# Performance work log

Hardware: AMD Instinct MI355X
Metric: run time of the kernel (lower is better)

Reference implementation:

```python
import jax, jax.numpy as jnp
import numpy as np

B, I, H = 8192, 1024, 2048
G = 2            # number of groups
WR = 256         # wRank
URANKS = [128, 128]


def setup_inputs() -> dict:
    key = jax.random.key(0)
    ks = jax.random.split(key, 7)
    Hg = H // G
    x = jax.random.normal(ks[0], (B, I), jnp.float32)
    h = jax.random.normal(ks[1], (B, H), jnp.float32)
    c = jax.random.normal(ks[2], (B, H), jnp.float32)
    W = 0.1 * jax.random.normal(ks[3], (I, WR), jnp.float32)
    # Ws[k]: (wRank, H) for k in {forget, input, out, gate}
    Ws = 0.1 * jax.random.normal(ks[4], (4, WR, H), jnp.float32)
    # Ug[idx][0]: (G, H/G, r) shared first factor per rotation idx
    U0 = 0.1 * jax.random.normal(ks[5], (len(URANKS), G, Hg, URANKS[0]), jnp.float32)
    # Ug[idx][1..4]: (G, r, H/G) per-gate second factors, order [f, i, o, g]
    Ugates = 0.1 * jax.random.normal(ks[6], (len(URANKS), 4, G, URANKS[0], Hg), jnp.float32)
    # biases init to ones in the original module; order [f, i, o, c]
    biases = jnp.ones((4, H), jnp.float32)
    return {"x": x, "h": h, "c": c, "W": W, "Ws": Ws,
            "U0": U0, "Ugates": Ugates, "biases": biases}


def _cell(x, h, c, W, Ws, U0, Ugates, biases):
    Bb, Hh = h.shape
    Hg = Hh // G
    # shared input projection: x @ W, then all 4 gate matrices at once
    xw = x @ W                                   # (B, WR)
    wVals = jnp.einsum('br,krh->kbh', xw, Ws)    # (4, B, H)
    hview = h.reshape(Bb, G, Hg)                 # (B, G, H/G)
    uVals = jnp.zeros_like(wVals)
    for idx in range(U0.shape[0]):
        # group rotation: index = [idx, idx+1, ..., 0, ..., idx-1]
        rolled = jnp.roll(hview, -idx, axis=1)                     # (B, G, H/G)
        t = jnp.einsum('bgk,gkr->bgr', rolled, U0[idx])            # shared first bmm
        uVals = uVals + jnp.einsum('bgr,fgrk->fbgk', t, Ugates[idx]).reshape(4, Bb, Hh)
    pre = wVals + uVals + biases[:, None, :]     # (4, B, H)
    f = jax.nn.sigmoid(pre[0])
    i = jax.nn.sigmoid(pre[1])
    o = jax.nn.sigmoid(pre[2])
    g = jnp.tanh(pre[3])
    c_next = f * c + i * g
    h_next = o * jnp.tanh(c_next)
    return c_next, h_next


def reference(x, h, c, W, Ws, U0, Ugates, biases):
    return _cell(x, h, c, W, Ws, U0, Ugates, biases)
```

## Files before the change

### kernel.cpp

```cpp
#include <hip/hip_runtime.h>
#include <math.h>


typedef _Float16 half_t;
typedef _Float16 half8 __attribute__((ext_vector_type(8)));
typedef float floatx4 __attribute__((ext_vector_type(4)));

#define MFMA16(a, b, c) __builtin_amdgcn_mfma_f32_16x16x32_f16((a), (b), (c), 0, 0, 0)

typedef __attribute__((address_space(3))) unsigned int lds_uint;
typedef __attribute__((address_space(1))) const unsigned int glb_uint;

__device__ __forceinline__ void gload_lds16(const void* gptr, void* ldsptr) {
    __builtin_amdgcn_global_load_lds((glb_uint*)gptr, (lds_uint*)ldsptr, 16, 0, 0);
}

__device__ __forceinline__ int swz_ro(int row, int lq) {
    return row * 32 + ((lq ^ ((row >> 1) & 3)) << 3);
}

#define OFF_VTH  0u
#define OFF_VTL  4194304u
#define OFF_WTH  8388608u
#define OFF_WTL  8650752u
#define OFF_U0TH 8912896u
#define OFF_U0TL 9437184u
#define OFF_ZH   9961472u
#define OFF_ZL   16252928u

__global__ void prep_Vt(const float* __restrict__ Ws, const float* __restrict__ Ug,
                        half_t* __restrict__ Vth, half_t* __restrict__ Vtl) {
    __shared__ half_t Lh[16][520];
    __shared__ half_t Ll[16][520];
    const int b   = blockIdx.x;
    const int f   = b & 3;
    const int hc4 = (b >> 2) & 3;
    const int hc6 = (b >> 4) & 15;
    const int g   = b >> 8;
    const int t   = threadIdx.x;
    const int kk  = t >> 4;
    const int hcl = t & 15;
    const int n   = hc6 * 64 + hc4 * 16 + hcl;

    for (int p = 0; p < 32; ++p) {
        const int k = p * 16 + kk;
        float v;
        if (k < 256)
            v = Ws[((size_t)f * 256 + k) * 2048 + g * 1024 + n];
        else if (k < 384)
            v = Ug[(((size_t)f * 2 + g) * 128 + (k - 256)) * 1024 + n];
        else
            v = Ug[(((size_t)(4 + f) * 2 + g) * 128 + (k - 384)) * 1024 + n];
        const half_t hi = (half_t)v;
        Lh[hcl][k] = hi;
        Ll[hcl][k] = (half_t)(v - (float)hi);
    }
    __syncthreads();
    const int rl = t >> 4;
    const int ch = (t & 15) * 32;
    const size_t R0 = (size_t)b * 16;
    half_t* dh = Vth + (R0 + rl) * 512 + ch;
    half_t* dl = Vtl + (R0 + rl) * 512 + ch;
#pragma unroll
    for (int j = 0; j < 4; ++j) {
        *(half8*)&dh[j * 8] = *(const half8*)&Lh[rl][ch + j * 8];
        *(half8*)&dl[j * 8] = *(const half8*)&Ll[rl][ch + j * 8];
    }
}

__global__ void prep_ABw(const float* __restrict__ W, const float* __restrict__ U0,
                         half_t* __restrict__ Wth, half_t* __restrict__ Wtl,
                         half_t* __restrict__ U0th, half_t* __restrict__ U0tl) {
    __shared__ half_t Lh[8][1040];
    __shared__ half_t Ll[8][1040];
    const int rb  = blockIdx.x;
    const int tgt = blockIdx.y;
    const int t   = threadIdx.x;
    const int kk  = t >> 3;
    const int rl  = t & 7;
    const int r   = rb * 8 + rl;

    for (int p = 0; p < 32; ++p) {
        const int k = p * 32 + kk;
        float v;
        if (tgt == 0) {
            v = W[(size_t)k * 256 + r];
        } else {
            const int jj = tgt - 1;
            if (r < 128) v = U0[((size_t)jj * 1024 + k) * 128 + r];
            else         v = U0[((size_t)(2 + (1 - jj)) * 1024 + k) * 128 + (r - 128)];
        }
        const half_t hi = (half_t)v;
        Lh[rl][k] = hi;
        Ll[rl][k] = (half_t)(v - (float)hi);
    }
    __syncthreads();
    const int orl = t >> 5;
    const int ch  = (t & 31) * 32;
    half_t *dh, *dl;
    if (tgt == 0) { dh = Wth; dl = Wtl; }
    else { dh = U0th + (size_t)(tgt - 1) * 262144; dl = U0tl + (size_t)(tgt - 1) * 262144; }
    dh += (size_t)(rb * 8 + orl) * 1024 + ch;
    dl += (size_t)(rb * 8 + orl) * 1024 + ch;
#pragma unroll
    for (int j = 0; j < 4; ++j) {
        *(half8*)&dh[j * 8] = *(const half8*)&Lh[orl][ch + j * 8];
        *(half8*)&dl[j * 8] = *(const half8*)&Ll[orl][ch + j * 8];
    }
}

__global__ __launch_bounds__(256, 2) void stageA_mfma(
    const float* __restrict__ x, const float* __restrict__ h,
    const half_t* __restrict__ Wth, const half_t* __restrict__ Wtl,
    const half_t* __restrict__ U0th, const half_t* __restrict__ U0tl,
    half_t* __restrict__ Zh, half_t* __restrict__ Zl) {
    __shared__ half_t Ah[64 * 32], Al[64 * 32];
    __shared__ half_t Bh[256 * 32], Bl[256 * 32];
    const int m0  = blockIdx.x * 64;
    const int seg = blockIdx.y;
    const int tid = threadIdx.x;
    const int l   = tid & 63, wid = tid >> 6;
    const int wr  = wid >> 1, wcn = wid & 1;

    const float* Asrc; int ldA;
    if (seg == 0) { Asrc = x; ldA = 1024; }
    else          { Asrc = h + (seg - 1) * 1024; ldA = 2048; }
    const half_t *Bsh, *Bsl;
    if (seg == 0) { Bsh = Wth; Bsl = Wtl; }
    else { Bsh = U0th + (size_t)(seg - 1) * 262144; Bsl = U0tl + (size_t)(seg - 1) * 262144; }

    const int arow = tid >> 2, au = tid & 3;
    const int aqp  = (au ^ ((tid >> 3) & 3));
    const float* aptr = Asrc + (size_t)(m0 + arow) * ldA + au * 8;
    const int lrow = l >> 2;
    const int lks  = ((l & 3) ^ ((l >> 3) & 3)) << 3;

    floatx4 acc[2][8] = {};

#pragma unroll 1
    for (int kt = 0; kt < 1024; kt += 32) {
        __syncthreads();
        const float4 v0 = *(const float4*)(aptr + kt);
        const float4 v1 = *(const float4*)(aptr + kt + 4);
        const float va[8] = {v0.x, v0.y, v0.z, v0.w, v1.x, v1.y, v1.z, v1.w};
        half8 hv, lv;
#pragma unroll
        for (int j = 0; j < 8; ++j) {
            const half_t hi = (half_t)va[j];
            hv[j] = hi;
            lv[j] = (half_t)(va[j] - (float)hi);
        }
        *(half8*)&Ah[arow * 32 + aqp * 8] = hv;
        *(half8*)&Al[arow * 32 + aqp * 8] = lv;
#pragma unroll
        for (int q = 0; q < 4; ++q) {
            const int i = wid * 4 + q;
            const size_t grow = (size_t)(i * 16 + lrow) * 1024 + kt + lks;
            gload_lds16(Bsh + grow, &Bh[i * 512]);
            gload_lds16(Bsl + grow, &Bl[i * 512]);
        }
        __syncthreads();

        half8 ah[2], al[2];
#pragma unroll
        for (int mt = 0; mt < 2; ++mt) {
            const int ro = swz_ro(wr * 32 + mt * 16 + (l & 15), l >> 4);
            ah[mt] = *(const half8*)&Ah[ro];
            al[mt] = *(const half8*)&Al[ro];
        }
#pragma unroll
        for (int nt = 0; nt < 8; ++nt) {
            const int ro = swz_ro(wcn * 128 + nt * 16 + (l & 15), l >> 4);
            const half8 bh = *(const half8*)&Bh[ro];
            const half8 bl = *(const half8*)&Bl[ro];
#pragma unroll
            for (int mt = 0; mt < 2; ++mt) {
                acc[mt][nt] = MFMA16(ah[mt], bh, acc[mt][nt]);
                acc[mt][nt] = MFMA16(ah[mt], bl, acc[mt][nt]);
                acc[mt][nt] = MFMA16(al[mt], bh, acc[mt][nt]);
            }
        }
    }
#pragma unroll
    for (int mt = 0; mt < 2; ++mt)
#pragma unroll
        for (int nt = 0; nt < 8; ++nt)
#pragma unroll
            for (int r = 0; r < 4; ++r) {
                const int row = m0 + wr * 32 + mt * 16 + (l >> 4) * 4 + r;
                const int col = seg * 256 + wcn * 128 + nt * 16 + (l & 15);
                const float v = acc[mt][nt][r];
                const half_t hi = (half_t)v;
                Zh[(size_t)row * 768 + col] = hi;
                Zl[(size_t)row * 768 + col] = (half_t)(v - (float)hi);
            }
}

__global__ __launch_bounds__(256, 2) void stageB_mfma(
    const half_t* __restrict__ Vth, const half_t* __restrict__ Vtl,
    const half_t* __restrict__ Zh, const half_t* __restrict__ Zl,
    const float* __restrict__ bias, const float* __restrict__ c,
    float* __restrict__ out) {
    __shared__ half_t Wh[256 * 32], Wl[256 * 32];
    __shared__ half_t Th[128 * 32], Tl[128 * 32];
    const int m0  = blockIdx.x * 128;
    const int hc6 = blockIdx.y;
    const int g   = blockIdx.z;
    const int tid = threadIdx.x;
    const int l   = tid & 63, wid = tid >> 6;
    const int wr  = wid >> 1, wc = wid & 1;
    const size_t vbase = ((size_t)g * 16 + hc6) * 256;
    const int lrow = l >> 2;
    const int lks  = ((l & 3) ^ ((l >> 3) & 3)) << 3;

    floatx4 acc[8][4] = {};

#pragma unroll 1
    for (int kt = 0; kt < 512; kt += 32) {
        const int zcol = (kt < 256) ? kt : ((kt < 384) ? kt + (g << 8) : kt + ((1 - g) << 8));
        __syncthreads();
#pragma unroll
        for (int q = 0; q < 4; ++q) {
            const int i = wid * 4 + q;
            const size_t grow = (vbase + i * 16 + lrow) * 512 + kt + lks;
            gload_lds16(Vth + grow, &Wh[i * 512]);
            gload_lds16(Vtl + grow, &Wl[i * 512]);
        }
#pragma unroll
        for (int q = 0; q < 2; ++q) {
            const int i = wid * 2 + q;
            const size_t grow = (size_t)(m0 + i * 16 + lrow) * 768 + zcol + lks;
            gload_lds16(Zh + grow, &Th[i * 512]);
            gload_lds16(Zl + grow, &Tl[i * 512]);
        }
        __syncthreads();

        half8 bh[4], bl[4];
#pragma unroll
        for (int mt = 0; mt < 4; ++mt) {
            const int ro = swz_ro(wc * 64 + mt * 16 + (l & 15), l >> 4);
            bh[mt] = *(const half8*)&Th[ro];
            bl[mt] = *(const half8*)&Tl[ro];
        }
#pragma unroll
        for (int nt = 0; nt < 8; ++nt) {
            const int ro = swz_ro(wr * 128 + nt * 16 + (l & 15), l >> 4);
            const half8 afh = *(const half8*)&Wh[ro];
            const half8 afl = *(const half8*)&Wl[ro];
#pragma unroll
            for (int mt = 0; mt < 4; ++mt) {
                acc[nt][mt] = MFMA16(afh, bh[mt], acc[nt][mt]);
                acc[nt][mt] = MFMA16(afh, bl[mt], acc[nt][mt]);
                acc[nt][mt] = MFMA16(afl, bh[mt], acc[nt][mt]);
            }
        }
    }

    const size_t outH = (size_t)8192 * 2048;
#pragma unroll
    for (int h4 = 0; h4 < 2; ++h4)
#pragma unroll
        for (int r = 0; r < 4; ++r) {
            const int hc   = hc6 * 64 + (wr * 2 + h4) * 16 + (l >> 4) * 4 + r;
            const int hcol = g * 1024 + hc;
            const float bf = bias[hcol];
            const float bi = bias[2048 + hcol];
            const float bo = bias[4096 + hcol];
            const float bg = bias[6144 + hcol];
#pragma unroll
            for (int mt = 0; mt < 4; ++mt) {
                const int m = m0 + wc * 64 + mt * 16 + (l & 15);
                const float pf = acc[h4 * 4 + 0][mt][r] + bf;
                const float pi = acc[h4 * 4 + 1][mt][r] + bi;
                const float po = acc[h4 * 4 + 2][mt][r] + bo;
                const float pg = acc[h4 * 4 + 3][mt][r] + bg;
                const float fg = 1.f / (1.f + __expf(-pf));
                const float ig = 1.f / (1.f + __expf(-pi));
                const float og = 1.f / (1.f + __expf(-po));
                const float gg = 2.f / (1.f + __expf(-2.f * pg)) - 1.f;
                const float cv = c[(size_t)m * 2048 + hcol];
                const float cn = fg * cv + ig * gg;
                const float th = 2.f / (1.f + __expf(-2.f * cn)) - 1.f;
                out[(size_t)m * 2048 + hcol]        = cn;
                out[outH + (size_t)m * 2048 + hcol] = og * th;
            }
        }
}

extern "C" void kernel_launch(void* const* d_in, const int* in_sizes, int n_in,
                              void* d_out, int out_size, void* d_ws, size_t ws_size,
                              hipStream_t stream) {
    const float* x    = (const float*)d_in[0];
    const float* h    = (const float*)d_in[1];
    const float* c    = (const float*)d_in[2];
    const float* W    = (const float*)d_in[3];
    const float* Ws   = (const float*)d_in[4];
    const float* U0   = (const float*)d_in[5];
    const float* Ug   = (const float*)d_in[6];
    const float* bias = (const float*)d_in[7];
    float* out = (float*)d_out;

    half_t* wsp  = (half_t*)d_ws;
    half_t* Vth  = wsp + OFF_VTH;
    half_t* Vtl  = wsp + OFF_VTL;
    half_t* Wth  = wsp + OFF_WTH;
    half_t* Wtl  = wsp + OFF_WTL;
    half_t* U0th = wsp + OFF_U0TH;
    half_t* U0tl = wsp + OFF_U0TL;
    half_t* Zh   = wsp + OFF_ZH;
    half_t* Zl   = wsp + OFF_ZL;

    prep_Vt<<<512, 256, 0, stream>>>(Ws, Ug, Vth, Vtl);
    prep_ABw<<<dim3(32, 3), 256, 0, stream>>>(W, U0, Wth, Wtl, U0th, U0tl);
    stageA_mfma<<<dim3(128, 3), 256, 0, stream>>>(x, h, Wth, Wtl, U0th, U0tl, Zh, Zl);
    stageB_mfma<<<dim3(64, 16, 2), 256, 0, stream>>>(Vth, Vtl, Zh, Zl, bias, c, out);
}
```

Measured before the change: 617.4 us.

## Triple-buffer stage B loads, widen to 512 threads, vectorize epilogue, prefetch A

Stage B moves to 512-thread blocks with 8 waves, each holding a smaller accumulator tile. Its global-to-LDS loads now run through a 3-stage ring buffer with explicit vmcnt waits, raw barriers and s_setprio around the MFMA loop, so memory latency overlaps compute. Blocks are remapped into a 1D grid with a swizzled order to improve L2 locality. The epilogue reads bias and c and writes outputs as float4, and stage A prefetches the next fp32 A tile into registers before it is needed. In exchange, LDS use and register pressure rise, and the hand-counted vmcnt values must match the exact number of loads issued per stage.

```diff
diff --git a/kernel.cpp b/kernel.cpp
--- a/kernel.cpp
+++ b/kernel.cpp
@@ -137,27 +137,32 @@
 
     floatx4 acc[2][8] = {};
 
+    float4 v0 = *(const float4*)(aptr);
+    float4 v1 = *(const float4*)(aptr + 4);
+
 #pragma unroll 1
     for (int kt = 0; kt < 1024; kt += 32) {
         __syncthreads();
-        const float4 v0 = *(const float4*)(aptr + kt);
-        const float4 v1 = *(const float4*)(aptr + kt + 4);
-        const float va[8] = {v0.x, v0.y, v0.z, v0.w, v1.x, v1.y, v1.z, v1.w};
-        half8 hv, lv;
-#pragma unroll
-        for (int j = 0; j < 8; ++j) {
-            const half_t hi = (half_t)va[j];
-            hv[j] = hi;
-            lv[j] = (half_t)(va[j] - (float)hi);
-        }
-        *(half8*)&Ah[arow * 32 + aqp * 8] = hv;
-        *(half8*)&Al[arow * 32 + aqp * 8] = lv;
 #pragma unroll
         for (int q = 0; q < 4; ++q) {
             const int i = wid * 4 + q;
             const size_t grow = (size_t)(i * 16 + lrow) * 1024 + kt + lks;
             gload_lds16(Bsh + grow, &Bh[i * 512]);
             gload_lds16(Bsl + grow, &Bl[i * 512]);
+        }
+        const float va[8] = {v0.x, v0.y, v0.z, v0.w, v1.x, v1.y, v1.z, v1.w};
+        half8 hv, lv;
+#pragma unroll
+        for (int j = 0; j < 8; ++j) {
+            const half_t hi = (half_t)va[j];
+            hv[j] = hi;
+            lv[j] = (half_t)(va[j] - (float)hi);
+        }
+        *(half8*)&Ah[arow * 32 + aqp * 8] = hv;
+        *(half8*)&Al[arow * 32 + aqp * 8] = lv;
+        if (kt + 32 < 1024) {
+            v0 = *(const float4*)(aptr + kt + 32);
+            v1 = *(const float4*)(aptr + kt + 36);
         }
         __syncthreads();
 
@@ -196,95 +201,128 @@
             }
 }
 
-__global__ __launch_bounds__(256, 2) void stageB_mfma(
+__global__ __launch_bounds__(512, 2) void stageB_mfma(
     const half_t* __restrict__ Vth, const half_t* __restrict__ Vtl,
     const half_t* __restrict__ Zh, const half_t* __restrict__ Zl,
     const float* __restrict__ bias, const float* __restrict__ c,
     float* __restrict__ out) {
-    __shared__ half_t Wh[256 * 32], Wl[256 * 32];
-    __shared__ half_t Th[128 * 32], Tl[128 * 32];
-    const int m0  = blockIdx.x * 128;
-    const int hc6 = blockIdx.y;
-    const int g   = blockIdx.z;
+    __shared__ half_t lds[3 * 24576];
     const int tid = threadIdx.x;
     const int l   = tid & 63, wid = tid >> 6;
-    const int wr  = wid >> 1, wc = wid & 1;
+    const int wr  = wid >> 2, wc = wid & 3;
+
+    const int lin = (blockIdx.x & 7) * 256 + (blockIdx.x >> 3);
+    const int mb  = lin >> 5;
+    const int rem = lin & 31;
+    const int g   = rem >> 4, hc6 = rem & 15;
+    const int m0  = mb * 128;
     const size_t vbase = ((size_t)g * 16 + hc6) * 256;
     const int lrow = l >> 2;
     const int lks  = ((l & 3) ^ ((l >> 3) & 3)) << 3;
 
-    floatx4 acc[8][4] = {};
-
-#pragma unroll 1
-    for (int kt = 0; kt < 512; kt += 32) {
+    auto stage = [&](int s) {
+        const int kt   = s * 32;
         const int zcol = (kt < 256) ? kt : ((kt < 384) ? kt + (g << 8) : kt + ((1 - g) << 8));
-        __syncthreads();
-#pragma unroll
-        for (int q = 0; q < 4; ++q) {
-            const int i = wid * 4 + q;
-            const size_t grow = (vbase + i * 16 + lrow) * 512 + kt + lks;
-            gload_lds16(Vth + grow, &Wh[i * 512]);
-            gload_lds16(Vtl + grow, &Wl[i * 512]);
-        }
+        half_t* base = &lds[(s % 3) * 24576];
 #pragma unroll
         for (int q = 0; q < 2; ++q) {
             const int i = wid * 2 + q;
-            const size_t grow = (size_t)(m0 + i * 16 + lrow) * 768 + zcol + lks;
-            gload_lds16(Zh + grow, &Th[i * 512]);
-            gload_lds16(Zl + grow, &Tl[i * 512]);
-        }
-        __syncthreads();
-
-        half8 bh[4], bl[4];
-#pragma unroll
-        for (int mt = 0; mt < 4; ++mt) {
-            const int ro = swz_ro(wc * 64 + mt * 16 + (l & 15), l >> 4);
-            bh[mt] = *(const half8*)&Th[ro];
-            bl[mt] = *(const half8*)&Tl[ro];
-        }
+            const size_t grow = (vbase + i * 16 + lrow) * 512 + kt + lks;
+            gload_lds16(Vth + grow, base + i * 512);
+        }
+#pragma unroll
+        for (int q = 0; q < 2; ++q) {
+            const int i = wid * 2 + q;
+            const size_t grow = (vbase + i * 16 + lrow) * 512 + kt + lks;
+            gload_lds16(Vtl + grow, base + 8192 + i * 512);
+        }
+        {
+            const size_t grow = (size_t)(m0 + wid * 16 + lrow) * 768 + zcol + lks;
+            gload_lds16(Zh + grow, base + 16384 + wid * 512);
+            gload_lds16(Zl + grow, base + 20480 + wid * 512);
+        }
+    };
+
+    floatx4 acc[8][2] = {};
+
+    stage(0);
+    stage(1);
+#pragma unroll 1
+    for (int s = 0; s < 16; ++s) {
+        if (s < 14) {
+            stage(s + 2);
+            asm volatile("s_waitcnt vmcnt(12)" ::: "memory");
+        } else if (s == 14) {
+            asm volatile("s_waitcnt vmcnt(6)" ::: "memory");
+        } else {
+            asm volatile("s_waitcnt vmcnt(0)" ::: "memory");
+        }
+        __builtin_amdgcn_s_barrier();
+
+        const half_t* base = &lds[(s % 3) * 24576];
+        half8 bh[2], bl[2];
+#pragma unroll
+        for (int mt = 0; mt < 2; ++mt) {
+            const int ro = swz_ro(wc * 32 + mt * 16 + (l & 15), l >> 4);
+            bh[mt] = *(const half8*)&base[16384 + ro];
+            bl[mt] = *(const half8*)&base[20480 + ro];
+        }
+        __builtin_amdgcn_s_setprio(1);
 #pragma unroll
         for (int nt = 0; nt < 8; ++nt) {
             const int ro = swz_ro(wr * 128 + nt * 16 + (l & 15), l >> 4);
-            const half8 afh = *(const half8*)&Wh[ro];
-            const half8 afl = *(const half8*)&Wl[ro];
-#pragma unroll
-            for (int mt = 0; mt < 4; ++mt) {
-                acc[nt][mt] = MFMA16(afh, bh[mt], acc[nt][mt]);
-                acc[nt][mt] = MFMA16(afh, bl[mt], acc[nt][mt]);
-                acc[nt][mt] = MFMA16(afl, bh[mt], acc[nt][mt]);
+            const half8 ah = *(const half8*)&base[ro];
+            const half8 al = *(const half8*)&base[8192 + ro];
+#pragma unroll
+            for (int mt = 0; mt < 2; ++mt) {
+                acc[nt][mt] = MFMA16(ah, bh[mt], acc[nt][mt]);
+                acc[nt][mt] = MFMA16(ah, bl[mt], acc[nt][mt]);
+                acc[nt][mt] = MFMA16(al, bh[mt], acc[nt][mt]);
             }
         }
+        __builtin_amdgcn_s_setprio(0);
+        __builtin_amdgcn_s_barrier();
     }
 
     const size_t outH = (size_t)8192 * 2048;
 #pragma unroll
-    for (int h4 = 0; h4 < 2; ++h4)
-#pragma unroll
-        for (int r = 0; r < 4; ++r) {
-            const int hc   = hc6 * 64 + (wr * 2 + h4) * 16 + (l >> 4) * 4 + r;
-            const int hcol = g * 1024 + hc;
-            const float bf = bias[hcol];
-            const float bi = bias[2048 + hcol];
-            const float bo = bias[4096 + hcol];
-            const float bg = bias[6144 + hcol];
-#pragma unroll
-            for (int mt = 0; mt < 4; ++mt) {
-                const int m = m0 + wc * 64 + mt * 16 + (l & 15);
-                const float pf = acc[h4 * 4 + 0][mt][r] + bf;
-                const float pi = acc[h4 * 4 + 1][mt][r] + bi;
-                const float po = acc[h4 * 4 + 2][mt][r] + bo;
-                const float pg = acc[h4 * 4 + 3][mt][r] + bg;
+    for (int h4 = 0; h4 < 2; ++h4) {
+        const int hbase = g * 1024 + hc6 * 64 + (wr * 2 + h4) * 16 + (l >> 4) * 4;
+        const float4 b0 = *(const float4*)(bias + 0 * 2048 + hbase);
+        const float4 b1 = *(const float4*)(bias + 1 * 2048 + hbase);
+        const float4 b2 = *(const float4*)(bias + 2 * 2048 + hbase);
+        const float4 b3 = *(const float4*)(bias + 3 * 2048 + hbase);
+        const float* b0p = (const float*)&b0;
+        const float* b1p = (const float*)&b1;
+        const float* b2p = (const float*)&b2;
+        const float* b3p = (const float*)&b3;
+#pragma unroll
+        for (int mt = 0; mt < 2; ++mt) {
+            const int m = m0 + wc * 32 + mt * 16 + (l & 15);
+            const float4 cv = *(const float4*)(c + (size_t)m * 2048 + hbase);
+            const float* cvp = (const float*)&cv;
+            float4 co, ho;
+            float* cop = (float*)&co;
+            float* hop = (float*)&ho;
+#pragma unroll
+            for (int r = 0; r < 4; ++r) {
+                const float pf = acc[h4 * 4 + 0][mt][r] + b0p[r];
+                const float pi = acc[h4 * 4 + 1][mt][r] + b1p[r];
+                const float po = acc[h4 * 4 + 2][mt][r] + b2p[r];
+                const float pg = acc[h4 * 4 + 3][mt][r] + b3p[r];
                 const float fg = 1.f / (1.f + __expf(-pf));
                 const float ig = 1.f / (1.f + __expf(-pi));
                 const float og = 1.f / (1.f + __expf(-po));
                 const float gg = 2.f / (1.f + __expf(-2.f * pg)) - 1.f;
-                const float cv = c[(size_t)m * 2048 + hcol];
-                const float cn = fg * cv + ig * gg;
+                const float cn = fg * cvp[r] + ig * gg;
                 const float th = 2.f / (1.f + __expf(-2.f * cn)) - 1.f;
-                out[(size_t)m * 2048 + hcol]        = cn;
-                out[outH + (size_t)m * 2048 + hcol] = og * th;
+                cop[r] = cn;
+                hop[r] = og * th;
             }
-        }
+            *(float4*)(out +        (size_t)m * 2048 + hbase) = co;
+            *(float4*)(out + outH + (size_t)m * 2048 + hbase) = ho;
+        }
+    }
 }
 
 extern "C" void kernel_launch(void* const* d_in, const int* in_sizes, int n_in,
@@ -313,5 +351,5 @@
     prep_Vt<<<512, 256, 0, stream>>>(Ws, Ug, Vth, Vtl);
     prep_ABw<<<dim3(32, 3), 256, 0, stream>>>(W, U0, Wth, Wtl, U0th, U0tl);
     stageA_mfma<<<dim3(128, 3), 256, 0, stream>>>(x, h, Wth, Wtl, U0th, U0tl, Zh, Zl);
-    stageB_mfma<<<dim3(64, 16, 2), 256, 0, stream>>>(Vth, Vtl, Zh, Zl, bias, c, out);
-}
+    stageB_mfma<<<2048, 512, 0, stream>>>(Vth, Vtl, Zh, Zl, bias, c, out);
+}
```

Result: faster. 568.7 us (-7.9%).
